# Kernel optimization log

Hardware: AMD Instinct MI355X
Metric: run time of the kernel (lower is better)

The kernel has to match this reference:

```python
import jax, jax.numpy as jnp
import numpy as np


def setup_inputs() -> dict:
    key = jax.random.key(0)
    ks = jax.random.split(key, 7)
    B, T, C, H = 4, 4096, 1024, 64
    x = jax.random.normal(ks[0], (B, T, C), dtype=jnp.float32)
    Wq = jax.random.normal(ks[1], (C, H), dtype=jnp.float32) * 0.02
    bq = jax.random.normal(ks[2], (H,), dtype=jnp.float32) * 0.02
    Wk = jax.random.normal(ks[3], (C, H), dtype=jnp.float32) * 0.02
    bk = jax.random.normal(ks[4], (H,), dtype=jnp.float32) * 0.02
    Wv = jax.random.normal(ks[5], (C, H), dtype=jnp.float32) * 0.02
    bv = jax.random.normal(ks[6], (H,), dtype=jnp.float32) * 0.02
    return {"x": x, "Wq": Wq, "bq": bq, "Wk": Wk, "bk": bk, "Wv": Wv, "bv": bv}


def reference(x, Wq, bq, Wk, bk, Wv, bv):
    B, T, C = x.shape
    q = x @ Wq + bq            # [B,T,H]
    k = x @ Wk + bk            # [B,T,H]
    v = x @ Wv + bv            # [B,T,H]
    # NOTE: original scales by C**-0.5 where C = n_embd (input dim), not head_size
    scale = jnp.asarray(C, x.dtype) ** -0.5
    wei = jnp.einsum('bth,bsh->bts', q, k) * scale   # [B,T,T]
    causal = jnp.tril(jnp.ones((T, T), dtype=bool))
    wei = jnp.where(causal, wei, -jnp.inf)
    wei = jax.nn.softmax(wei, axis=-1)
    out = jnp.einsum('bts,bsh->bth', wei, v)         # [B,T,H]
    return out
```

## Files before the change

kernel.cpp:

```cpp
#include <hip/hip_runtime.h>
#include <hip/hip_bf16.h>

#define T_DIM 4096
#define C_DIM 1024
#define H_DIM 64
#define B_DIM 4

typedef __attribute__((ext_vector_type(8))) short short8v;
typedef __attribute__((ext_vector_type(4))) short short4v;
typedef __attribute__((ext_vector_type(4))) float float4v;

__device__ __forceinline__ unsigned short f2bf(float f) {
    __hip_bfloat16 h = __float2bfloat16(f);
    return *reinterpret_cast<unsigned short*>(&h);
}
__device__ __forceinline__ float bf2f(unsigned short u) {
    __hip_bfloat16 h = *reinterpret_cast<__hip_bfloat16*>(&u);
    return __bfloat162float(h);
}

__device__ __forceinline__ int vperm(int t5) {
    return ((t5 & 12) << 1) | (t5 & 3) | ((t5 & 16) >> 2);
}

__device__ __forceinline__ int chunk_prefix(int t) {
    const int g = t >> 3;
    return t + 4 * g * (g - 1) + (t & 7) * g;
}

#define GLL16(gsrc, ldst)                                                         \
    __builtin_amdgcn_global_load_lds(                                             \
        (const __attribute__((address_space(1))) unsigned int*)(gsrc),            \
        (__attribute__((address_space(3))) unsigned int*)(ldst), 16, 0, 0)

__global__ __launch_bounds__(256) void wprep(
    const float* __restrict__ Wq, const float* __restrict__ Wk,
    const float* __restrict__ Wv, unsigned short* __restrict__ wt)
{
    __shared__ float tile[64][65];
    const int t  = threadIdx.x;
    const int m  = blockIdx.x >> 4;
    const int k0 = (blockIdx.x & 15) * 64;
    const float* __restrict__ W = (m == 0) ? Wq : (m == 1) ? Wk : Wv;

    const int kr = t >> 4, c4 = (t & 15) * 4;
#pragma unroll
    for (int j = 0; j < 4; ++j) {
        const int row = kr + j * 16;
        const float4 v = *(const float4*)(W + (size_t)(k0 + row) * 64 + c4);
        tile[row][c4 + 0] = v.x; tile[row][c4 + 1] = v.y;
        tile[row][c4 + 2] = v.z; tile[row][c4 + 3] = v.w;
    }
    __syncthreads();

    const int col = t >> 2, q = t & 3;
    short8v s0, s1;
#pragma unroll
    for (int j = 0; j < 8; ++j) s0[j] = (short)f2bf(tile[q * 16 + j][col]);
#pragma unroll
    for (int j = 0; j < 8; ++j) s1[j] = (short)f2bf(tile[q * 16 + 8 + j][col]);
    unsigned short* dst = wt + (size_t)(m * 64 + col) * 1024 + k0 + q * 16;
    *(short8v*)dst = s0;
    *(short8v*)(dst + 8) = s1;
}

__global__ __launch_bounds__(512, 2) void qkv_gemm(
    const float* __restrict__ x, const unsigned short* __restrict__ wt,
    const float* __restrict__ bq, const float* __restrict__ bk,
    const float* __restrict__ bv,
    unsigned short* __restrict__ qb, unsigned short* __restrict__ kmat,
    unsigned short* __restrict__ vP)
{
    __shared__ __align__(16) unsigned char lx[2][4096];
    __shared__ __align__(16) unsigned char lw[3][24576];

    const int t    = threadIdx.x;
    const int lane = t & 63;
    const int w    = t >> 6;
    const int l15  = lane & 15;
    const int g4   = lane >> 4;
    const int r0   = blockIdx.x * 32;

    const int rg  = w & 1;
    const int cgr = (w >> 1) & 1;
    const int kh  = w >> 2;

    const int srow  = t >> 4;
    const int sq    = t & 15;
    const int xbyte = srow * 128 + ((sq >> 1) ^ (srow & 7)) * 16 + (sq & 1) * 8;
    const float* __restrict__ xsrc = x + (size_t)(r0 + srow) * C_DIM + sq * 4;
    const int wgs = (t & 7) ^ ((t >> 3) & 7);
    const unsigned char* __restrict__ wB = (const unsigned char*)wt;

    float4v acc[6];
#pragma unroll
    for (int cg = 0; cg < 6; ++cg) acc[cg] = (float4v){0.f, 0.f, 0.f, 0.f};

#define WSTAGE(p, kb)                                                             \
    {                                                                             \
        _Pragma("unroll")                                                         \
        for (int i = 0; i < 3; ++i)                                               \
            GLL16(wB + (size_t)(i * 64 + (t >> 3)) * 2048 + (kb) * 128 + wgs * 16,\
                  &lw[p][(i * 512 + t) * 16]);                                    \
    }
#define XCVT_WRITE(p, v)                                                          \
    {                                                                             \
        __hip_bfloat162 c0_ = __float22bfloat162_rn(make_float2((v).x, (v).y));   \
        __hip_bfloat162 c1_ = __float22bfloat162_rn(make_float2((v).z, (v).w));   \
        unsigned int* d_ = (unsigned int*)&lx[p][xbyte];                          \
        d_[0] = *(unsigned int*)&c0_;                                             \
        d_[1] = *(unsigned int*)&c1_;                                             \
    }

    float4 xv[3];

    {
        const float4 x0 = *(const float4*)xsrc;
        XCVT_WRITE(0, x0);
        __builtin_amdgcn_sched_barrier(0);
        WSTAGE(0, 0);
        WSTAGE(1, 1);
        __builtin_amdgcn_sched_barrier(0);
        xv[1] = *(const float4*)(xsrc + 64);
        xv[2] = *(const float4*)(xsrc + 128);
        asm volatile("s_waitcnt vmcnt(5) lgkmcnt(0)" ::: "memory");
        __builtin_amdgcn_s_barrier();
    }

    const int arow = rg * 16 + l15;
    const int axor = arow & 7;
    const int kg   = kh * 4 + g4;

#pragma unroll
    for (int kb = 0; kb < 14; ++kb) {
        WSTAGE((kb + 2) % 3, kb + 2);
        __builtin_amdgcn_sched_barrier(0);
        const int d = (kb + 3 < 16) ? (kb + 3) : 15;
        xv[kb % 3] = *(const float4*)(xsrc + d * 64);

        const short8v af = *(const short8v*)&lx[kb & 1][arow * 128 + (kg ^ axor) * 16];
#pragma unroll
        for (int cg = 0; cg < 6; ++cg) {
            const int col = cgr * 96 + cg * 16 + l15;
            const short8v bf =
                *(const short8v*)&lw[kb % 3][col * 128 + ((kg ^ (col & 7))) * 16];
            acc[cg] = __builtin_amdgcn_mfma_f32_16x16x32_bf16(af, bf, acc[cg], 0, 0, 0);
        }

        XCVT_WRITE((kb + 1) & 1, xv[(kb + 1) % 3]);
        asm volatile("s_waitcnt vmcnt(5) lgkmcnt(0)" ::: "memory");
        __builtin_amdgcn_s_barrier();
    }
    {
        const short8v af = *(const short8v*)&lx[0][arow * 128 + (kg ^ axor) * 16];
#pragma unroll
        for (int cg = 0; cg < 6; ++cg) {
            const int col = cgr * 96 + cg * 16 + l15;
            const short8v bf =
                *(const short8v*)&lw[2][col * 128 + ((kg ^ (col & 7))) * 16];
            acc[cg] = __builtin_amdgcn_mfma_f32_16x16x32_bf16(af, bf, acc[cg], 0, 0, 0);
        }
        XCVT_WRITE(1, xv[0]);
        asm volatile("s_waitcnt vmcnt(0) lgkmcnt(0)" ::: "memory");
        __builtin_amdgcn_s_barrier();
    }
    {
        const short8v af = *(const short8v*)&lx[1][arow * 128 + (kg ^ axor) * 16];
#pragma unroll
        for (int cg = 0; cg < 6; ++cg) {
            const int col = cgr * 96 + cg * 16 + l15;
            const short8v bf =
                *(const short8v*)&lw[0][col * 128 + ((kg ^ (col & 7))) * 16];
            acc[cg] = __builtin_amdgcn_mfma_f32_16x16x32_bf16(af, bf, acc[cg], 0, 0, 0);
        }
    }
    __syncthreads();

    float* comm = (float*)lw;
    if (kh == 1) {
        const int base = ((w - 4) * 64 + lane) * 24;
#pragma unroll
        for (int cg = 0; cg < 6; ++cg)
#pragma unroll
            for (int e = 0; e < 4; ++e) comm[base + cg * 4 + e] = acc[cg][e];
    }
    __syncthreads();
    if (kh == 0) {
        const int base = (w * 64 + lane) * 24;
#pragma unroll
        for (int cg = 0; cg < 6; ++cg)
#pragma unroll
            for (int e = 0; e < 4; ++e) acc[cg][e] += comm[base + cg * 4 + e];

        const float qs = 0.03125f * 1.44269504088896f;
#pragma unroll
        for (int cg = 0; cg < 6; ++cg) {
            const int cabs = cgr * 96 + cg * 16 + l15;
            const int m    = cabs >> 6;
            const int h    = cabs & 63;
            const float bb = ((m == 0) ? bq : (m == 1) ? bk : bv)[h];
#pragma unroll
            for (int rr = 0; rr < 4; ++rr) {
                const int row = r0 + rg * 16 + 4 * g4 + rr;
                const float vv = acc[cg][rr] + bb;
                if (m == 0) {
                    qb[(size_t)row * 64 + h] = f2bf(vv * qs);
                } else if (m == 1) {
                    kmat[(size_t)row * 64 + h] = f2bf(vv);
                } else {
                    const int b_i = row >> 12;
                    const int tt  = row & 4095;
                    const int tp  = (tt & ~31) | vperm(tt & 31);
                    vP[((size_t)b_i * 64 + h) * T_DIM + tp] = f2bf(vv);
                }
            }
        }
    }
#undef WSTAGE
#undef XCVT_WRITE
}

__global__ __launch_bounds__(256, 4) void attn_part(
    const unsigned short* __restrict__ qb, const unsigned short* __restrict__ kmat,
    const unsigned short* __restrict__ vP, unsigned short* __restrict__ pO,
    float* __restrict__ pl)
{
    __shared__ __align__(16) unsigned char lk[3][4096];
    __shared__ __align__(16) unsigned char lv[3][4096];

    const int tid  = threadIdx.x;
    const int w    = tid >> 6;
    const int lane = tid & 63;
    const int l15  = lane & 15;
    const int g    = lane >> 4;

    const int b   = blockIdx.x & 3;
    const int idx = 287 - (blockIdx.x >> 2);
    int t = 0;
    for (int tt = 1; tt < 64; ++tt)
        if (chunk_prefix(tt) <= idx) t = tt;
    const int c    = idx - chunk_prefix(t);
    const int q0   = t * 64;
    const int kv_l = q0 + 64;
    const int d0   = c * 512;
    const int dend = (d0 + 512 < kv_l) ? (d0 + 512) : kv_l;
    const int ns   = (dend - d0) >> 5;
    const int slot = b * 288 + idx;

    const unsigned char* kB = (const unsigned char*)kmat + (size_t)b * T_DIM * 128;
    const unsigned char* vB = (const unsigned char*)vP + (size_t)b * 64 * T_DIM * 2;
    const int krow = tid >> 3, kdg = tid & 7;
    const int vh = tid >> 2, vdg = tid & 3;
    const unsigned char* ksrc = kB + krow * 128 + ((kdg ^ (krow & 7)) * 16);
    const unsigned char* vsrc = vB + (size_t)vh * 8192 + ((vdg ^ (vh & 3)) * 16);
    const int kdst = tid * 16;

#define STAGE(p, ss)                                                          \
    {                                                                         \
        const int off_ = d0 + (ss) * 32;                                      \
        GLL16(ksrc + (size_t)off_ * 128, &lk[p][kdst]);                       \
        GLL16(vsrc + (size_t)off_ * 2,   &lv[p][kdst]);                       \
    }

    const unsigned short* qrow = qb + ((size_t)b * T_DIM + q0 + 16 * w + l15) * 64;
    const short8v qf0 = *(const short8v*)(qrow + 8 * g);
    const short8v qf1 = *(const short8v*)(qrow + 32 + 8 * g);

    short8v kones;
#pragma unroll
    for (int j = 0; j < 8; ++j) kones[j] = (short)0x3F80;

    float4v acc[4];
    float4v accl = (float4v){0.f, 0.f, 0.f, 0.f};
#pragma unroll
    for (int f = 0; f < 4; ++f) acc[f] = (float4v){0.f, 0.f, 0.f, 0.f};

    const int qmax = q0 + 16 * w + 15;
    const int kxor = l15 & 7;
    const int vxor = l15 & 3;

    STAGE(0, 0);
    STAGE(1, (ns > 1) ? 1 : 0);
    asm volatile("s_waitcnt vmcnt(2)" ::: "memory");
    __builtin_amdgcn_s_barrier();

    int p = 0;
    for (int s = 0; s < ns; ++s) {
        const int ps = (p + 2 >= 3) ? (p - 1) : (p + 2);
        const int sn = (s + 2 < ns) ? (s + 2) : (ns - 1);
        STAGE(ps, sn);

        const int kv0 = d0 + s * 32;
        if (kv0 <= qmax) {
            const short8v ka0 = *(const short8v*)&lk[p][(l15 * 8 + (g ^ kxor)) * 16];
            const short8v ka1 = *(const short8v*)&lk[p][(l15 * 8 + ((4 + g) ^ kxor)) * 16];
            const short8v ka2 = *(const short8v*)&lk[p][((16 + l15) * 8 + (g ^ kxor)) * 16];
            const short8v ka3 = *(const short8v*)&lk[p][((16 + l15) * 8 + ((4 + g) ^ kxor)) * 16];
            short8v vb[4];
#pragma unroll
            for (int f = 0; f < 4; ++f)
                vb[f] = *(const short8v*)&lv[p][((f * 16 + l15) * 4 + (g ^ vxor)) * 16];

            const float4v z = (float4v){0.f, 0.f, 0.f, 0.f};
            float4v slo = __builtin_amdgcn_mfma_f32_16x16x32_bf16(ka0, qf0, z, 0, 0, 0);
            slo = __builtin_amdgcn_mfma_f32_16x16x32_bf16(ka1, qf1, slo, 0, 0, 0);
            float4v shi = __builtin_amdgcn_mfma_f32_16x16x32_bf16(ka2, qf0, z, 0, 0, 0);
            shi = __builtin_amdgcn_mfma_f32_16x16x32_bf16(ka3, qf1, shi, 0, 0, 0);

            float pl_[4], ph_[4];
            if (kv0 + 31 <= q0 + 16 * w) {
#pragma unroll
                for (int r = 0; r < 4; ++r) {
                    pl_[r] = exp2f(slo[r]);
                    ph_[r] = exp2f(shi[r]);
                }
            } else {
                const int qabs = q0 + 16 * w + l15;
#pragma unroll
                for (int r = 0; r < 4; ++r) {
                    const int kvlo = kv0 + 4 * g + r;
                    pl_[r] = (kvlo <= qabs) ? exp2f(slo[r]) : 0.f;
                    ph_[r] = (kvlo + 16 <= qabs) ? exp2f(shi[r]) : 0.f;
                }
            }
            short8v pa;
            {
                unsigned int* pu = (unsigned int*)&pa;
                __hip_bfloat162 c0 = __float22bfloat162_rn(make_float2(pl_[0], pl_[1]));
                __hip_bfloat162 c1 = __float22bfloat162_rn(make_float2(pl_[2], pl_[3]));
                __hip_bfloat162 c2 = __float22bfloat162_rn(make_float2(ph_[0], ph_[1]));
                __hip_bfloat162 c3 = __float22bfloat162_rn(make_float2(ph_[2], ph_[3]));
                pu[0] = *(unsigned int*)&c0;
                pu[1] = *(unsigned int*)&c1;
                pu[2] = *(unsigned int*)&c2;
                pu[3] = *(unsigned int*)&c3;
            }
#pragma unroll
            for (int f = 0; f < 4; ++f)
                acc[f] = __builtin_amdgcn_mfma_f32_16x16x32_bf16(pa, vb[f], acc[f], 0, 0, 0);
            accl = __builtin_amdgcn_mfma_f32_16x16x32_bf16(pa, kones, accl, 0, 0, 0);
        }

        asm volatile("s_waitcnt vmcnt(2) lgkmcnt(0)" ::: "memory");
        __builtin_amdgcn_s_barrier();
        p = (p + 1 >= 3) ? 0 : (p + 1);
    }

    unsigned short* po = pO + (size_t)slot * 4096 + (size_t)(16 * w) * 64;
#pragma unroll
    for (int f = 0; f < 4; ++f)
#pragma unroll
        for (int r = 0; r < 4; ++r)
            po[(4 * g + r) * 64 + f * 16 + l15] = f2bf(acc[f][r]);
    if (l15 == 0) {
#pragma unroll
        for (int r = 0; r < 4; ++r)
            pl[(size_t)slot * 64 + 16 * w + 4 * g + r] = accl[r];
    }
#undef STAGE
}

__global__ __launch_bounds__(256) void attn_comb(
    const unsigned short* __restrict__ pO, const float* __restrict__ pl,
    float* __restrict__ out)
{
    const int tid  = blockIdx.x * 256 + threadIdx.x;
    const int row  = tid >> 4;
    const int h4   = (tid & 15) * 4;
    const int b    = row >> 12;
    const int brow = row & 4095;
    const int t    = brow >> 6;
    const int rr   = brow & 63;
    const int nc   = 1 + (t >> 3);
    const int base = b * 288 + chunk_prefix(t);

    const unsigned short* src = pO + (size_t)base * 4096 + rr * 64 + h4;
    const float* lsrc = pl + (size_t)base * 64 + rr;
    float4 o = make_float4(0.f, 0.f, 0.f, 0.f);
    float l = 0.f;
    for (int c = 0; c < nc; ++c) {
        const short4v s = *(const short4v*)(src + (size_t)c * 4096);
        o.x += bf2f((unsigned short)s[0]);
        o.y += bf2f((unsigned short)s[1]);
        o.z += bf2f((unsigned short)s[2]);
        o.w += bf2f((unsigned short)s[3]);
        l += lsrc[(size_t)c * 64];
    }
    const float inv = 1.f / l;
    o.x *= inv; o.y *= inv; o.z *= inv; o.w *= inv;
    *(float4*)(out + (size_t)row * 64 + h4) = o;
}

extern "C" void kernel_launch(void* const* d_in, const int* in_sizes, int n_in,
                              void* d_out, int out_size, void* d_ws, size_t ws_size,
                              hipStream_t stream) {
    const float* x  = (const float*)d_in[0];
    const float* Wq = (const float*)d_in[1];
    const float* bq = (const float*)d_in[2];
    const float* Wk = (const float*)d_in[3];
    const float* bk = (const float*)d_in[4];
    const float* Wv = (const float*)d_in[5];
    const float* bv = (const float*)d_in[6];
    float* out = (float*)d_out;

    char* ws = (char*)d_ws;
    unsigned short* qb   = (unsigned short*)(ws);
    unsigned short* kmat = (unsigned short*)(ws + (2u << 20));
    unsigned short* vP   = (unsigned short*)(ws + (4u << 20));
    unsigned short* wt   = (unsigned short*)(ws + (6u << 20));
    unsigned short* pO   = (unsigned short*)(ws + (8u << 20));
    float*          pl   = (float*)(ws + (8u << 20) + 9437184u);

    wprep<<<48, 256, 0, stream>>>(Wq, Wk, Wv, wt);
    qkv_gemm<<<512, 512, 0, stream>>>(x, wt, bq, bk, bv, qb, kmat, vP);
    attn_part<<<1152, 256, 0, stream>>>(qb, kmat, vP, pO, pl);
    attn_comb<<<1024, 256, 0, stream>>>(pO, pl, out);
}
```

Baseline: 55.52 us.

## Load x directly into MFMA A-fragments, dropping the LDS staging buffer

The QKV GEMM stops staging x through a swizzled LDS buffer. Each lane now loads its own 8 fp32 values of the A fragment straight from global memory into registers, with a three-deep register prefetch, and packs them to bf16 for the MFMA. This removes the LDS writes and reads for x and frees 8KB of shared memory, so launch bounds are raised to 4 blocks per CU for more occupancy. In exchange the global loads for x are less coalesced, since each lane reads 32 bytes with a 4KB row stride, and the waitcnt counts had to be retuned, which is fragile.

```diff
diff --git a/kernel.cpp b/kernel.cpp
--- a/kernel.cpp
+++ b/kernel.cpp
@@ -17,6 +17,20 @@
 __device__ __forceinline__ float bf2f(unsigned short u) {
     __hip_bfloat16 h = *reinterpret_cast<__hip_bfloat16*>(&u);
     return __bfloat162float(h);
+}
+
+__device__ __forceinline__ short8v pack8(float4 a, float4 b) {
+    short8v r;
+    unsigned int* u = (unsigned int*)&r;
+    __hip_bfloat162 c0 = __float22bfloat162_rn(make_float2(a.x, a.y));
+    __hip_bfloat162 c1 = __float22bfloat162_rn(make_float2(a.z, a.w));
+    __hip_bfloat162 c2 = __float22bfloat162_rn(make_float2(b.x, b.y));
+    __hip_bfloat162 c3 = __float22bfloat162_rn(make_float2(b.z, b.w));
+    u[0] = *(unsigned int*)&c0;
+    u[1] = *(unsigned int*)&c1;
+    u[2] = *(unsigned int*)&c2;
+    u[3] = *(unsigned int*)&c3;
+    return r;
 }
 
 __device__ __forceinline__ int vperm(int t5) {
@@ -64,14 +78,13 @@
     *(short8v*)(dst + 8) = s1;
 }
 
-__global__ __launch_bounds__(512, 2) void qkv_gemm(
+__global__ __launch_bounds__(512, 4) void qkv_gemm(
     const float* __restrict__ x, const unsigned short* __restrict__ wt,
     const float* __restrict__ bq, const float* __restrict__ bk,
     const float* __restrict__ bv,
     unsigned short* __restrict__ qb, unsigned short* __restrict__ kmat,
     unsigned short* __restrict__ vP)
 {
-    __shared__ __align__(16) unsigned char lx[2][4096];
     __shared__ __align__(16) unsigned char lw[3][24576];
 
     const int t    = threadIdx.x;
@@ -85,10 +98,10 @@
     const int cgr = (w >> 1) & 1;
     const int kh  = w >> 2;
 
-    const int srow  = t >> 4;
-    const int sq    = t & 15;
-    const int xbyte = srow * 128 + ((sq >> 1) ^ (srow & 7)) * 16 + (sq & 1) * 8;
-    const float* __restrict__ xsrc = x + (size_t)(r0 + srow) * C_DIM + sq * 4;
+    const int kg   = kh * 4 + g4;
+    const float* __restrict__ xrow =
+        x + (size_t)(r0 + rg * 16 + l15) * C_DIM + kg * 8;
+
     const int wgs = (t & 7) ^ ((t >> 3) & 7);
     const unsigned char* __restrict__ wB = (const unsigned char*)wt;
 
@@ -103,42 +116,29 @@
             GLL16(wB + (size_t)(i * 64 + (t >> 3)) * 2048 + (kb) * 128 + wgs * 16,\
                   &lw[p][(i * 512 + t) * 16]);                                    \
     }
-#define XCVT_WRITE(p, v)                                                          \
-    {                                                                             \
-        __hip_bfloat162 c0_ = __float22bfloat162_rn(make_float2((v).x, (v).y));   \
-        __hip_bfloat162 c1_ = __float22bfloat162_rn(make_float2((v).z, (v).w));   \
-        unsigned int* d_ = (unsigned int*)&lx[p][xbyte];                          \
-        d_[0] = *(unsigned int*)&c0_;                                             \
-        d_[1] = *(unsigned int*)&c1_;                                             \
-    }
-
-    float4 xv[3];
+
+    float4 xv[3][2];
 
     {
-        const float4 x0 = *(const float4*)xsrc;
-        XCVT_WRITE(0, x0);
-        __builtin_amdgcn_sched_barrier(0);
         WSTAGE(0, 0);
         WSTAGE(1, 1);
         __builtin_amdgcn_sched_barrier(0);
-        xv[1] = *(const float4*)(xsrc + 64);
-        xv[2] = *(const float4*)(xsrc + 128);
-        asm volatile("s_waitcnt vmcnt(5) lgkmcnt(0)" ::: "memory");
+        xv[0][0] = *(const float4*)(xrow);
+        xv[0][1] = *(const float4*)(xrow + 4);
+        xv[1][0] = *(const float4*)(xrow + 64);
+        xv[1][1] = *(const float4*)(xrow + 68);
+        asm volatile("s_waitcnt vmcnt(7) lgkmcnt(0)" ::: "memory");
         __builtin_amdgcn_s_barrier();
     }
-
-    const int arow = rg * 16 + l15;
-    const int axor = arow & 7;
-    const int kg   = kh * 4 + g4;
 
 #pragma unroll
     for (int kb = 0; kb < 14; ++kb) {
         WSTAGE((kb + 2) % 3, kb + 2);
         __builtin_amdgcn_sched_barrier(0);
-        const int d = (kb + 3 < 16) ? (kb + 3) : 15;
-        xv[kb % 3] = *(const float4*)(xsrc + d * 64);
-
-        const short8v af = *(const short8v*)&lx[kb & 1][arow * 128 + (kg ^ axor) * 16];
+        xv[(kb + 2) % 3][0] = *(const float4*)(xrow + (kb + 2) * 64);
+        xv[(kb + 2) % 3][1] = *(const float4*)(xrow + (kb + 2) * 64 + 4);
+
+        const short8v af = pack8(xv[kb % 3][0], xv[kb % 3][1]);
 #pragma unroll
         for (int cg = 0; cg < 6; ++cg) {
             const int col = cgr * 96 + cg * 16 + l15;
@@ -147,12 +147,11 @@
             acc[cg] = __builtin_amdgcn_mfma_f32_16x16x32_bf16(af, bf, acc[cg], 0, 0, 0);
         }
 
-        XCVT_WRITE((kb + 1) & 1, xv[(kb + 1) % 3]);
-        asm volatile("s_waitcnt vmcnt(5) lgkmcnt(0)" ::: "memory");
+        asm volatile("s_waitcnt vmcnt(7) lgkmcnt(0)" ::: "memory");
         __builtin_amdgcn_s_barrier();
     }
     {
-        const short8v af = *(const short8v*)&lx[0][arow * 128 + (kg ^ axor) * 16];
+        const short8v af = pack8(xv[2][0], xv[2][1]);
 #pragma unroll
         for (int cg = 0; cg < 6; ++cg) {
             const int col = cgr * 96 + cg * 16 + l15;
@@ -160,12 +159,11 @@
                 *(const short8v*)&lw[2][col * 128 + ((kg ^ (col & 7))) * 16];
             acc[cg] = __builtin_amdgcn_mfma_f32_16x16x32_bf16(af, bf, acc[cg], 0, 0, 0);
         }
-        XCVT_WRITE(1, xv[0]);
-        asm volatile("s_waitcnt vmcnt(0) lgkmcnt(0)" ::: "memory");
+        asm volatile("s_waitcnt vmcnt(2) lgkmcnt(0)" ::: "memory");
         __builtin_amdgcn_s_barrier();
     }
     {
-        const short8v af = *(const short8v*)&lx[1][arow * 128 + (kg ^ axor) * 16];
+        const short8v af = pack8(xv[0][0], xv[0][1]);
 #pragma unroll
         for (int cg = 0; cg < 6; ++cg) {
             const int col = cgr * 96 + cg * 16 + l15;
@@ -217,7 +215,6 @@
         }
     }
 #undef WSTAGE
-#undef XCVT_WRITE
 }
 
 __global__ __launch_bounds__(256, 4) void attn_part(
```

Measured after the change: 63.65 us. +14.6%, slower.
